# Kernel optimization log

Hardware: AMD Instinct MI355X
Metric: run time of the kernel (lower is better)

The kernel has to match this reference:

```python
import jax, jax.numpy as jnp
import numpy as np

N = 50000          # nodes
E = 600000         # edges
D = 128            # g_dim = h1_dim = h2_dim
R = 8              # 2 * n_speakers**2, n_speakers=2
B = 10             # num_bases


def setup_inputs() -> dict:
    key = jax.random.key(0)
    ks = jax.random.split(key, 10)
    s = 1.0 / np.sqrt(D)
    return {
        "node_features": jax.random.normal(ks[0], (N, D), jnp.float32),
        "edge_index": jax.random.randint(ks[1], (2, E), 0, N, jnp.int64),
        "edge_type": jax.random.randint(ks[2], (E,), 0, R, jnp.int64),
        # RGCNConv params (basis decomposition)
        "basis": jax.random.normal(ks[3], (B, D, D), jnp.float32) * s,
        "comp": jax.random.normal(ks[4], (R, B), jnp.float32) * (1.0 / np.sqrt(B)),
        "root": jax.random.normal(ks[5], (D, D), jnp.float32) * s,
        "bias1": jnp.zeros((D,), jnp.float32),
        # GraphConv params
        "w_rel": jax.random.normal(ks[6], (D, D), jnp.float32) * s,
        "b_rel": jnp.zeros((D,), jnp.float32),
        "w_root": jax.random.normal(ks[7], (D, D), jnp.float32) * s,
    }


def reference(node_features, edge_index, edge_type, basis, comp, root, bias1, w_rel, b_rel, w_root):
    x = node_features
    n = x.shape[0]
    r = comp.shape[0]
    src, dst = edge_index[0], edge_index[1]

    # ---- RGCNConv (basis decomposition, per-relation mean aggregation) ----
    # project through bases once: [N, B, D]
    xb = jnp.einsum('ni,bio->nbo', x, basis)
    # per-edge message: combine bases with relation coefficients  [E, D]
    msg = jnp.einsum('eb,ebo->eo', comp[edge_type], xb[src])
    # per-(dst, relation) mean normalization
    seg = dst * r + edge_type                       # [E]
    cnt = jax.ops.segment_sum(jnp.ones((msg.shape[0],), x.dtype), seg, num_segments=n * r)
    norm = 1.0 / jnp.maximum(cnt[seg], 1.0)         # [E]
    agg = jax.ops.segment_sum(msg * norm[:, None], dst, num_segments=n)  # [N, D]
    h1 = agg + x @ root + bias1

    # ---- GraphConv (add aggregation of neighbors + root transform) ----
    nbr = jax.ops.segment_sum(h1[src], dst, num_segments=n)  # [N, D]
    out = nbr @ w_rel.T + b_rel + h1 @ w_root.T
    return out
```

## Files before the change

kernel.cpp:

```cpp
#include <hip/hip_runtime.h>
#include <stdint.h>

#define N_NODES 50000
#define E_EDGES 600000
#define D 128
#define R_REL 8
#define B_BASES 10
#define RN (R_REL * N_NODES)

typedef __attribute__((ext_vector_type(8))) short bf16x8;
typedef __attribute__((ext_vector_type(4))) float f32x4;

__device__ __forceinline__ short f2b(float f) {
    uint32_t u = __float_as_uint(f);
    u += 0x7fff + ((u >> 16) & 1);
    return (short)(u >> 16);
}
__device__ __forceinline__ float b2f(uint16_t u) {
    return __uint_as_float((uint32_t)u << 16);
}

__global__ __launch_bounds__(256) void k_prep(const float* __restrict__ basis,
                                              const float* __restrict__ comp,
                                              const float* __restrict__ root,
                                              const float* __restrict__ wrel,
                                              const float* __restrict__ wroot,
                                              short* __restrict__ wt,
                                              short* __restrict__ wrel_b,
                                              short* __restrict__ wroot_b) {
    int tid = blockIdx.x * 256 + threadIdx.x;
    if (tid < 9 * D * D) {
        int s = tid >> 14;
        int rem = tid & 16383;
        int j = rem >> 7, i = rem & 127;
        float v;
        if (s < 8) {
            v = 0.f;
#pragma unroll
            for (int b = 0; b < B_BASES; b++)
                v += comp[s * B_BASES + b] * basis[b * D * D + i * D + j];
        } else {
            v = root[i * D + j];
        }
        wt[tid] = f2b(v);
    } else {
        int t2 = tid - 9 * D * D;
        if (t2 < D * D) {
            wrel_b[t2]  = f2b(wrel[t2]);
            wroot_b[t2] = f2b(wroot[t2]);
        }
    }
}

__global__ __launch_bounds__(256) void k_misc(const float* __restrict__ x,
                                              unsigned short* __restrict__ xb,
                                              const int* __restrict__ dst,
                                              const int* __restrict__ et,
                                              int* __restrict__ cntr) {
    int tid = blockIdx.x * 256 + threadIdx.x;
    if (tid < N_NODES * D / 8) {
        const float4* s = (const float4*)x + (size_t)tid * 2;
        float4 v0 = s[0], v1 = s[1];
        union { uint4 u; unsigned short h[8]; } pk;
        pk.h[0] = (unsigned short)f2b(v0.x); pk.h[1] = (unsigned short)f2b(v0.y);
        pk.h[2] = (unsigned short)f2b(v0.z); pk.h[3] = (unsigned short)f2b(v0.w);
        pk.h[4] = (unsigned short)f2b(v1.x); pk.h[5] = (unsigned short)f2b(v1.y);
        pk.h[6] = (unsigned short)f2b(v1.z); pk.h[7] = (unsigned short)f2b(v1.w);
        ((uint4*)xb)[tid] = pk.u;
    } else {
        int e = tid - N_NODES * D / 8;
        if (e < E_EDGES)
            atomicAdd(&cntr[dst[e] * R_REL + et[e]], 1);
    }
}

__device__ __forceinline__ int wave_scan_incl(int v) {
    int lane = threadIdx.x & 63;
#pragma unroll
    for (int off = 1; off < 64; off <<= 1) {
        int n = __shfl_up(v, off, 64);
        if (lane >= off) v += n;
    }
    return v;
}

__global__ __launch_bounds__(1024) void k_scan_a(const int* __restrict__ in,
                                                 int* __restrict__ out,
                                                 int* __restrict__ bsum, int n) {
    __shared__ int wsum[16];
    int t = threadIdx.x, lane = t & 63, wid = t >> 6;
    int g = blockIdx.x * 1024 + t;
    int v = (g < n) ? in[g] : 0;
    int isc = wave_scan_incl(v);
    if (lane == 63) wsum[wid] = isc;
    __syncthreads();
    if (wid == 0) {
        int wv = (lane < 16) ? wsum[lane] : 0;
        int wsc = wave_scan_incl(wv);
        if (lane < 16) wsum[lane] = wsc - wv;
    }
    __syncthreads();
    if (g < n) out[g] = wsum[wid] + isc - v;
    if (t == 1023 && bsum) bsum[blockIdx.x] = wsum[15] + isc;
}

__global__ __launch_bounds__(1024) void k_scan_c(int* __restrict__ out,
                                                 const int* __restrict__ bsum, int n) {
    int g = blockIdx.x * 1024 + threadIdx.x;
    if (g < n) out[g] += bsum[blockIdx.x];
}

__global__ __launch_bounds__(256) void k_bucket(const int* __restrict__ src,
                                                const int* __restrict__ dst,
                                                const int* __restrict__ et,
                                                const int* __restrict__ cntr,
                                                int* __restrict__ seg_off,
                                                int* __restrict__ es1,
                                                float* __restrict__ enorm) {
    int e = blockIdx.x * 256 + threadIdx.x;
    if (e >= E_EDGES) return;
    int r = et[e];
    int key = dst[e] * R_REL + r;
    int pos = atomicAdd(&seg_off[key], 1);
    es1[pos] = (src[e] << 3) | r;
    enorm[pos] = 1.0f / (float)cntr[key];
}

__global__ __launch_bounds__(256) void k_ygemm(const unsigned short* __restrict__ xb,
                                               const short* __restrict__ wt,
                                               unsigned short* __restrict__ ybig) {
    __shared__ short xs[64 * 128];
    __shared__ short ws[128 * 128];
    int slice = blockIdx.y;
    const short* w = wt + (size_t)slice * D * D;
    unsigned short* y = ybig + (size_t)slice * N_NODES * D;
    int base = blockIdx.x * 64;
    int t = threadIdx.x;
    const uint4* wsrc = (const uint4*)w;
    for (int idx = t; idx < 2048; idx += 256) {
        int j = idx >> 4, c = idx & 15;
        *(uint4*)&ws[j * 128 + ((c ^ (j & 15)) << 3)] = wsrc[idx];
    }
    for (int idx = t; idx < 1024; idx += 256) {
        int row = idx >> 4, c = idx & 15;
        int node = base + row;
        uint4 v = make_uint4(0, 0, 0, 0);
        if (node < N_NODES) v = ((const uint4*)(xb + (size_t)node * D))[c];
        *(uint4*)&xs[row * 128 + ((c ^ (row & 15)) << 3)] = v;
    }
    __syncthreads();

    int wave = t >> 6, lane = t & 63, quad = lane >> 4, l16 = lane & 15;
    f32x4 acc[8];
#pragma unroll
    for (int jt = 0; jt < 8; jt++) acc[jt] = (f32x4){0.f, 0.f, 0.f, 0.f};
#pragma unroll
    for (int kc = 0; kc < 4; kc++) {
        int c0 = kc * 4 + quad;
        bf16x8 a = *(const bf16x8*)&xs[(wave * 16 + l16) * 128 + ((c0 ^ l16) << 3)];
#pragma unroll
        for (int jt = 0; jt < 8; jt++) {
            bf16x8 b = *(const bf16x8*)&ws[(jt * 16 + l16) * 128 + ((c0 ^ l16) << 3)];
            acc[jt] = __builtin_amdgcn_mfma_f32_16x16x32_bf16(a, b, acc[jt], 0, 0, 0);
        }
    }
#pragma unroll
    for (int reg = 0; reg < 4; reg++) {
        int node = base + wave * 16 + quad * 4 + reg;
        if (node >= N_NODES) continue;
#pragma unroll
        for (int jt = 0; jt < 8; jt++)
            y[(size_t)node * D + jt * 16 + l16] = (unsigned short)f2b(acc[jt][reg]);
    }
}

__global__ __launch_bounds__(256) void k_agg8(const unsigned short* __restrict__ ybig,
                                              const int* __restrict__ es1,
                                              const float* __restrict__ enorm,
                                              const int* __restrict__ seg_off,
                                              const float* __restrict__ bias1,
                                              unsigned short* __restrict__ h1b) {
    int t = threadIdx.x;
    int wave = t >> 6, lane = t & 63, sub = lane >> 4, l = lane & 15;
    int d = blockIdx.x * 16 + wave * 4 + sub;
    if (d >= N_NODES) return;
    int start = (d == 0) ? 0 : seg_off[d * R_REL - 1];
    int end = seg_off[d * R_REL + 7];
    float acc[8];
#pragma unroll
    for (int j = 0; j < 8; j++) acc[j] = 0.f;
    size_t loff = (size_t)l * 8;

    int pos = start;
    for (; pos + 4 <= end; pos += 4) {
        int p0 = es1[pos], p1 = es1[pos + 1], p2 = es1[pos + 2], p3 = es1[pos + 3];
        float m0 = enorm[pos], m1 = enorm[pos + 1], m2 = enorm[pos + 2], m3 = enorm[pos + 3];
        uint4 v0 = *(const uint4*)(ybig + ((size_t)(p0 & 7) * N_NODES + (p0 >> 3)) * D + loff);
        uint4 v1 = *(const uint4*)(ybig + ((size_t)(p1 & 7) * N_NODES + (p1 >> 3)) * D + loff);
        uint4 v2 = *(const uint4*)(ybig + ((size_t)(p2 & 7) * N_NODES + (p2 >> 3)) * D + loff);
        uint4 v3 = *(const uint4*)(ybig + ((size_t)(p3 & 7) * N_NODES + (p3 >> 3)) * D + loff);
        const uint32_t* w0 = (const uint32_t*)&v0;
        const uint32_t* w1 = (const uint32_t*)&v1;
        const uint32_t* w2 = (const uint32_t*)&v2;
        const uint32_t* w3 = (const uint32_t*)&v3;
#pragma unroll
        for (int q = 0; q < 4; q++) {
            acc[q * 2]     += m0 * b2f((uint16_t)w0[q]) + m1 * b2f((uint16_t)w1[q]) +
                              m2 * b2f((uint16_t)w2[q]) + m3 * b2f((uint16_t)w3[q]);
            acc[q * 2 + 1] += m0 * b2f((uint16_t)(w0[q] >> 16)) + m1 * b2f((uint16_t)(w1[q] >> 16)) +
                              m2 * b2f((uint16_t)(w2[q] >> 16)) + m3 * b2f((uint16_t)(w3[q] >> 16));
        }
    }
    for (; pos < end; pos++) {
        int p0 = es1[pos];
        float m0 = enorm[pos];
        uint4 v0 = *(const uint4*)(ybig + ((size_t)(p0 & 7) * N_NODES + (p0 >> 3)) * D + loff);
        const uint32_t* w0 = (const uint32_t*)&v0;
#pragma unroll
        for (int q = 0; q < 4; q++) {
            acc[q * 2]     += m0 * b2f((uint16_t)w0[q]);
            acc[q * 2 + 1] += m0 * b2f((uint16_t)(w0[q] >> 16));
        }
    }

    uint4 rv = *(const uint4*)(ybig + ((size_t)8 * N_NODES + d) * D + loff);
    const uint32_t* rw = (const uint32_t*)&rv;
    float4 ba = *(const float4*)(bias1 + l * 8);
    float4 bb = *(const float4*)(bias1 + l * 8 + 4);
    float bv[8] = {ba.x, ba.y, ba.z, ba.w, bb.x, bb.y, bb.z, bb.w};
    union { uint4 u; unsigned short h[8]; } pk;
#pragma unroll
    for (int q = 0; q < 4; q++) {
        pk.h[q * 2]     = (unsigned short)f2b(acc[q * 2] + b2f((uint16_t)rw[q]) + bv[q * 2]);
        pk.h[q * 2 + 1] = (unsigned short)f2b(acc[q * 2 + 1] + b2f((uint16_t)(rw[q] >> 16)) + bv[q * 2 + 1]);
    }
    *(uint4*)(h1b + (size_t)d * D + loff) = pk.u;
}

__global__ __launch_bounds__(256) void k_agg_nbr(const unsigned short* __restrict__ h1b,
                                                 const int* __restrict__ es1,
                                                 const int* __restrict__ seg_off,
                                                 unsigned short* __restrict__ nbr) {
    int t = threadIdx.x;
    int wave = t >> 6, lane = t & 63, sub = lane >> 4, l = lane & 15;
    int d = blockIdx.x * 16 + wave * 4 + sub;
    if (d >= N_NODES) return;
    int start = (d == 0) ? 0 : seg_off[d * R_REL - 1];
    int end = seg_off[d * R_REL + 7];
    float acc[8];
#pragma unroll
    for (int j = 0; j < 8; j++) acc[j] = 0.f;
    size_t loff = (size_t)l * 8;

    int pos = start;
    for (; pos + 4 <= end; pos += 4) {
        int i0 = es1[pos] >> 3, i1 = es1[pos + 1] >> 3;
        int i2 = es1[pos + 2] >> 3, i3 = es1[pos + 3] >> 3;
        uint4 v0 = *(const uint4*)(h1b + (size_t)i0 * D + loff);
        uint4 v1 = *(const uint4*)(h1b + (size_t)i1 * D + loff);
        uint4 v2 = *(const uint4*)(h1b + (size_t)i2 * D + loff);
        uint4 v3 = *(const uint4*)(h1b + (size_t)i3 * D + loff);
        const uint32_t* w0 = (const uint32_t*)&v0;
        const uint32_t* w1 = (const uint32_t*)&v1;
        const uint32_t* w2 = (const uint32_t*)&v2;
        const uint32_t* w3 = (const uint32_t*)&v3;
#pragma unroll
        for (int q = 0; q < 4; q++) {
            acc[q * 2]     += b2f((uint16_t)w0[q]) + b2f((uint16_t)w1[q]) +
                              b2f((uint16_t)w2[q]) + b2f((uint16_t)w3[q]);
            acc[q * 2 + 1] += b2f((uint16_t)(w0[q] >> 16)) + b2f((uint16_t)(w1[q] >> 16)) +
                              b2f((uint16_t)(w2[q] >> 16)) + b2f((uint16_t)(w3[q] >> 16));
        }
    }
    for (; pos < end; pos++) {
        int i0 = es1[pos] >> 3;
        uint4 v0 = *(const uint4*)(h1b + (size_t)i0 * D + loff);
        const uint32_t* w0 = (const uint32_t*)&v0;
#pragma unroll
        for (int q = 0; q < 4; q++) {
            acc[q * 2]     += b2f((uint16_t)w0[q]);
            acc[q * 2 + 1] += b2f((uint16_t)(w0[q] >> 16));
        }
    }

    union { uint4 u; unsigned short h[8]; } pk;
#pragma unroll
    for (int j = 0; j < 8; j++) pk.h[j] = (unsigned short)f2b(acc[j]);
    *(uint4*)(nbr + (size_t)d * D + loff) = pk.u;
}

__global__ __launch_bounds__(256) void k_out2(const unsigned short* __restrict__ h1b,
                                              const unsigned short* __restrict__ nbr,
                                              const short* __restrict__ wroot_b,
                                              const short* __restrict__ wrel_b,
                                              const float* __restrict__ brel,
                                              float* __restrict__ out) {
    __shared__ short xs1[64 * 128];
    __shared__ short xs2[64 * 128];
    __shared__ short ws1[128 * 128];
    __shared__ short ws2[128 * 128];
    int base = blockIdx.x * 64;
    int t = threadIdx.x;
    const uint4* w1 = (const uint4*)wroot_b;
    const uint4* w2 = (const uint4*)wrel_b;
    for (int idx = t; idx < 2048; idx += 256) {
        int j = idx >> 4, c = idx & 15;
        int sw = j * 128 + ((c ^ (j & 15)) << 3);
        *(uint4*)&ws1[sw] = w1[idx];
        *(uint4*)&ws2[sw] = w2[idx];
    }
    for (int idx = t; idx < 1024; idx += 256) {
        int row = idx >> 4, c = idx & 15;
        int node = base + row;
        uint4 v1 = make_uint4(0, 0, 0, 0), v2 = make_uint4(0, 0, 0, 0);
        if (node < N_NODES) {
            v1 = ((const uint4*)(h1b + (size_t)node * D))[c];
            v2 = ((const uint4*)(nbr + (size_t)node * D))[c];
        }
        int sw = row * 128 + ((c ^ (row & 15)) << 3);
        *(uint4*)&xs1[sw] = v1;
        *(uint4*)&xs2[sw] = v2;
    }
    __syncthreads();

    int wave = t >> 6, lane = t & 63, quad = lane >> 4, l16 = lane & 15;
    f32x4 acc[8];
#pragma unroll
    for (int jt = 0; jt < 8; jt++) acc[jt] = (f32x4){0.f, 0.f, 0.f, 0.f};
#pragma unroll
    for (int kc = 0; kc < 4; kc++) {
        int c0 = kc * 4 + quad;
        int arow = (wave * 16 + l16) * 128 + ((c0 ^ l16) << 3);
        bf16x8 a1 = *(const bf16x8*)&xs1[arow];
        bf16x8 a2 = *(const bf16x8*)&xs2[arow];
#pragma unroll
        for (int jt = 0; jt < 8; jt++) {
            int brow = (jt * 16 + l16) * 128 + ((c0 ^ l16) << 3);
            bf16x8 b1 = *(const bf16x8*)&ws1[brow];
            bf16x8 b2 = *(const bf16x8*)&ws2[brow];
            acc[jt] = __builtin_amdgcn_mfma_f32_16x16x32_bf16(a1, b1, acc[jt], 0, 0, 0);
            acc[jt] = __builtin_amdgcn_mfma_f32_16x16x32_bf16(a2, b2, acc[jt], 0, 0, 0);
        }
    }
#pragma unroll
    for (int reg = 0; reg < 4; reg++) {
        int node = base + wave * 16 + quad * 4 + reg;
        if (node >= N_NODES) continue;
#pragma unroll
        for (int jt = 0; jt < 8; jt++) {
            int col = jt * 16 + l16;
            out[(size_t)node * D + col] = acc[jt][reg] + brel[col];
        }
    }
}

extern "C" void kernel_launch(void* const* d_in, const int* in_sizes, int n_in,
                              void* d_out, int out_size, void* d_ws, size_t ws_size,
                              hipStream_t stream) {
    const float* x     = (const float*)d_in[0];
    const int*   ei    = (const int*)d_in[1];
    const int*   et    = (const int*)d_in[2];
    const float* basis = (const float*)d_in[3];
    const float* comp  = (const float*)d_in[4];
    const float* root  = (const float*)d_in[5];
    const float* bias1 = (const float*)d_in[6];
    const float* wrel  = (const float*)d_in[7];
    const float* brel  = (const float*)d_in[8];
    const float* wroot = (const float*)d_in[9];
    float* out = (float*)d_out;
    const int* src = ei;
    const int* dst = ei + E_EDGES;

    char* p = (char*)d_ws;
    auto alloc = [&](size_t bytes) { char* q = p; p += (bytes + 255) & ~(size_t)255; return q; };
    short* wt      = (short*)alloc((size_t)9 * D * D * sizeof(short));
    short* wrel_b  = (short*)alloc(D * D * sizeof(short));
    short* wroot_b = (short*)alloc(D * D * sizeof(short));
    int*   cntr    = (int*)alloc((size_t)RN * sizeof(int));
    int*   seg_off = (int*)alloc((size_t)RN * sizeof(int));
    int*   es1     = (int*)alloc((size_t)(E_EDGES + 16) * sizeof(int));
    float* enorm   = (float*)alloc((size_t)(E_EDGES + 16) * sizeof(float));
    int*   bsum    = (int*)alloc(1024 * sizeof(int));
    unsigned short* xb   = (unsigned short*)alloc((size_t)N_NODES * D * sizeof(unsigned short));
    unsigned short* ybig = (unsigned short*)alloc((size_t)9 * N_NODES * D * sizeof(unsigned short));
    unsigned short* h1b  = (unsigned short*)alloc((size_t)N_NODES * D * sizeof(unsigned short));
    unsigned short* nbr  = xb;

    hipMemsetAsync(cntr, 0, (size_t)RN * sizeof(int), stream);

    k_prep<<<(9 * D * D + D * D + 255) / 256, 256, 0, stream>>>(
        basis, comp, root, wrel, wroot, wt, wrel_b, wroot_b);
    k_misc<<<(N_NODES * D / 8 + E_EDGES + 255) / 256, 256, 0, stream>>>(x, xb, dst, et, cntr);

    int nscan = (RN + 1023) / 1024;
    k_scan_a<<<nscan, 1024, 0, stream>>>(cntr, seg_off, bsum, RN);
    k_scan_a<<<1, 1024, 0, stream>>>(bsum, bsum, nullptr, nscan);
    k_scan_c<<<nscan, 1024, 0, stream>>>(seg_off, bsum, RN);

    k_bucket<<<(E_EDGES + 255) / 256, 256, 0, stream>>>(src, dst, et, cntr, seg_off, es1, enorm);

    int nb = (N_NODES + 63) / 64;
    int na = (N_NODES + 15) / 16;

    k_ygemm<<<dim3(nb, 9), 256, 0, stream>>>(xb, wt, ybig);
    k_agg8<<<na, 256, 0, stream>>>(ybig, es1, enorm, seg_off, bias1, h1b);
    k_agg_nbr<<<na, 256, 0, stream>>>(h1b, es1, seg_off, nbr);
    k_out2<<<nb, 256, 0, stream>>>(h1b, nbr, wroot_b, wrel_b, brel, out);
}
```

Before: 287.4 us.

## Aggregate before transform and fuse gather with MFMA GEMMs per node tile

Reorders the RGCN layer so that inputs are first mean-aggregated per relation, then each relation's weight is applied with MFMA inside one kernel. This removes the 9-slice projected tensor and its large write and read. The GraphConv neighbor sum is likewise fused into the output GEMM kernel, and the prep and misc launches are merged into one kernel. In exchange, each 64-node block gathers edges serially between GEMM passes and reloads a weight slice nine times, so memory latency and compute are less overlapped.

After: 348.7 us. 1.21x slower.

```diff
diff --git a/kernel.cpp b/kernel.cpp
--- a/kernel.cpp
+++ b/kernel.cpp
@@ -20,45 +20,22 @@
     return __uint_as_float((uint32_t)u << 16);
 }
 
-__global__ __launch_bounds__(256) void k_prep(const float* __restrict__ basis,
-                                              const float* __restrict__ comp,
-                                              const float* __restrict__ root,
-                                              const float* __restrict__ wrel,
-                                              const float* __restrict__ wroot,
-                                              short* __restrict__ wt,
-                                              short* __restrict__ wrel_b,
-                                              short* __restrict__ wroot_b) {
+__global__ __launch_bounds__(256) void k_front(const float* __restrict__ x,
+                                               unsigned short* __restrict__ xb,
+                                               const int* __restrict__ dst,
+                                               const int* __restrict__ et,
+                                               int* __restrict__ cntr,
+                                               const float* __restrict__ basis,
+                                               const float* __restrict__ comp,
+                                               const float* __restrict__ root,
+                                               const float* __restrict__ wrel,
+                                               const float* __restrict__ wroot,
+                                               short* __restrict__ wt,
+                                               short* __restrict__ wrel_b,
+                                               short* __restrict__ wroot_b) {
+    const int XB_N = N_NODES * D / 8;
     int tid = blockIdx.x * 256 + threadIdx.x;
-    if (tid < 9 * D * D) {
-        int s = tid >> 14;
-        int rem = tid & 16383;
-        int j = rem >> 7, i = rem & 127;
-        float v;
-        if (s < 8) {
-            v = 0.f;
-#pragma unroll
-            for (int b = 0; b < B_BASES; b++)
-                v += comp[s * B_BASES + b] * basis[b * D * D + i * D + j];
-        } else {
-            v = root[i * D + j];
-        }
-        wt[tid] = f2b(v);
-    } else {
-        int t2 = tid - 9 * D * D;
-        if (t2 < D * D) {
-            wrel_b[t2]  = f2b(wrel[t2]);
-            wroot_b[t2] = f2b(wroot[t2]);
-        }
-    }
-}
-
-__global__ __launch_bounds__(256) void k_misc(const float* __restrict__ x,
-                                              unsigned short* __restrict__ xb,
-                                              const int* __restrict__ dst,
-                                              const int* __restrict__ et,
-                                              int* __restrict__ cntr) {
-    int tid = blockIdx.x * 256 + threadIdx.x;
-    if (tid < N_NODES * D / 8) {
+    if (tid < XB_N) {
         const float4* s = (const float4*)x + (size_t)tid * 2;
         float4 v0 = s[0], v1 = s[1];
         union { uint4 u; unsigned short h[8]; } pk;
@@ -67,10 +44,32 @@
         pk.h[4] = (unsigned short)f2b(v1.x); pk.h[5] = (unsigned short)f2b(v1.y);
         pk.h[6] = (unsigned short)f2b(v1.z); pk.h[7] = (unsigned short)f2b(v1.w);
         ((uint4*)xb)[tid] = pk.u;
+    } else if (tid < XB_N + E_EDGES) {
+        int e = tid - XB_N;
+        atomicAdd(&cntr[dst[e] * R_REL + et[e]], 1);
     } else {
-        int e = tid - N_NODES * D / 8;
-        if (e < E_EDGES)
-            atomicAdd(&cntr[dst[e] * R_REL + et[e]], 1);
+        int t2 = tid - XB_N - E_EDGES;
+        if (t2 < 9 * D * D) {
+            int s = t2 >> 14;
+            int rem = t2 & 16383;
+            int j = rem >> 7, i = rem & 127;
+            float v;
+            if (s < 8) {
+                v = 0.f;
+#pragma unroll
+                for (int b = 0; b < B_BASES; b++)
+                    v += comp[s * B_BASES + b] * basis[b * D * D + i * D + j];
+            } else {
+                v = root[i * D + j];
+            }
+            wt[t2] = f2b(v);
+        } else {
+            int t3 = t2 - 9 * D * D;
+            if (t3 < D * D) {
+                wrel_b[t3]  = f2b(wrel[t3]);
+                wroot_b[t3] = f2b(wroot[t3]);
+            }
+        }
     }
 }
 
@@ -113,235 +112,213 @@
 __global__ __launch_bounds__(256) void k_bucket(const int* __restrict__ src,
                                                 const int* __restrict__ dst,
                                                 const int* __restrict__ et,
-                                                const int* __restrict__ cntr,
                                                 int* __restrict__ seg_off,
-                                                int* __restrict__ es1,
-                                                float* __restrict__ enorm) {
+                                                int* __restrict__ es1) {
     int e = blockIdx.x * 256 + threadIdx.x;
     if (e >= E_EDGES) return;
-    int r = et[e];
-    int key = dst[e] * R_REL + r;
+    int key = dst[e] * R_REL + et[e];
     int pos = atomicAdd(&seg_off[key], 1);
-    es1[pos] = (src[e] << 3) | r;
-    enorm[pos] = 1.0f / (float)cntr[key];
-}
-
-__global__ __launch_bounds__(256) void k_ygemm(const unsigned short* __restrict__ xb,
-                                               const short* __restrict__ wt,
-                                               unsigned short* __restrict__ ybig) {
+    es1[pos] = src[e];
+}
+
+__global__ __launch_bounds__(256) void k_h1_fused(const unsigned short* __restrict__ xb,
+                                                  const short* __restrict__ wt,
+                                                  const int* __restrict__ es1,
+                                                  const int* __restrict__ seg_off,
+                                                  const float* __restrict__ bias1,
+                                                  unsigned short* __restrict__ h1b) {
     __shared__ short xs[64 * 128];
     __shared__ short ws[128 * 128];
-    int slice = blockIdx.y;
-    const short* w = wt + (size_t)slice * D * D;
-    unsigned short* y = ybig + (size_t)slice * N_NODES * D;
+    __shared__ int sb[513];
     int base = blockIdx.x * 64;
     int t = threadIdx.x;
-    const uint4* wsrc = (const uint4*)w;
-    for (int idx = t; idx < 2048; idx += 256) {
-        int j = idx >> 4, c = idx & 15;
-        *(uint4*)&ws[j * 128 + ((c ^ (j & 15)) << 3)] = wsrc[idx];
-    }
-    for (int idx = t; idx < 1024; idx += 256) {
-        int row = idx >> 4, c = idx & 15;
-        int node = base + row;
-        uint4 v = make_uint4(0, 0, 0, 0);
-        if (node < N_NODES) v = ((const uint4*)(xb + (size_t)node * D))[c];
-        *(uint4*)&xs[row * 128 + ((c ^ (row & 15)) << 3)] = v;
-    }
-    __syncthreads();
+
+    for (int j = t; j < 513; j += 256) {
+        int g = base * 8 + j - 1;
+        sb[j] = (g < 0) ? 0 : seg_off[g < RN ? g : RN - 1];
+    }
 
     int wave = t >> 6, lane = t & 63, quad = lane >> 4, l16 = lane & 15;
+    int sw = t >> 4, l = t & 15;
     f32x4 acc[8];
 #pragma unroll
     for (int jt = 0; jt < 8; jt++) acc[jt] = (f32x4){0.f, 0.f, 0.f, 0.f};
-#pragma unroll
-    for (int kc = 0; kc < 4; kc++) {
-        int c0 = kc * 4 + quad;
-        bf16x8 a = *(const bf16x8*)&xs[(wave * 16 + l16) * 128 + ((c0 ^ l16) << 3)];
-#pragma unroll
-        for (int jt = 0; jt < 8; jt++) {
-            bf16x8 b = *(const bf16x8*)&ws[(jt * 16 + l16) * 128 + ((c0 ^ l16) << 3)];
-            acc[jt] = __builtin_amdgcn_mfma_f32_16x16x32_bf16(a, b, acc[jt], 0, 0, 0);
-        }
-    }
+
+    for (int r = 0; r < 9; r++) {
+        __syncthreads();
+        const uint4* wsrc = (const uint4*)(wt + (size_t)r * D * D);
+        for (int idx = t; idx < 2048; idx += 256) {
+            int j = idx >> 4, c = idx & 15;
+            *(uint4*)&ws[j * 128 + ((c ^ (j & 15)) << 3)] = wsrc[idx];
+        }
+        if (r < 8) {
+#pragma unroll
+            for (int ii = 0; ii < 4; ii++) {
+                int row = ii * 16 + sw;
+                int start = sb[row * 8 + r], end = sb[row * 8 + r + 1];
+                float ax[8];
+#pragma unroll
+                for (int q = 0; q < 8; q++) ax[q] = 0.f;
+                int pos = start;
+                for (; pos + 2 <= end; pos += 2) {
+                    int s0 = es1[pos], s1 = es1[pos + 1];
+                    uint4 v0 = *(const uint4*)(xb + (size_t)s0 * D + l * 8);
+                    uint4 v1 = *(const uint4*)(xb + (size_t)s1 * D + l * 8);
+                    const uint32_t* w0 = (const uint32_t*)&v0;
+                    const uint32_t* w1 = (const uint32_t*)&v1;
+#pragma unroll
+                    for (int q = 0; q < 4; q++) {
+                        ax[q * 2]     += b2f((uint16_t)w0[q]) + b2f((uint16_t)w1[q]);
+                        ax[q * 2 + 1] += b2f((uint16_t)(w0[q] >> 16)) + b2f((uint16_t)(w1[q] >> 16));
+                    }
+                }
+                if (pos < end) {
+                    int s0 = es1[pos];
+                    uint4 v0 = *(const uint4*)(xb + (size_t)s0 * D + l * 8);
+                    const uint32_t* w0 = (const uint32_t*)&v0;
+#pragma unroll
+                    for (int q = 0; q < 4; q++) {
+                        ax[q * 2]     += b2f((uint16_t)w0[q]);
+                        ax[q * 2 + 1] += b2f((uint16_t)(w0[q] >> 16));
+                    }
+                }
+                float nm = (end > start) ? 1.f / (float)(end - start) : 0.f;
+                union { uint4 u; unsigned short h[8]; } pk;
+#pragma unroll
+                for (int q = 0; q < 8; q++) pk.h[q] = (unsigned short)f2b(ax[q] * nm);
+                *(uint4*)&xs[row * 128 + ((l ^ (row & 15)) << 3)] = pk.u;
+            }
+        } else {
+            for (int idx = t; idx < 1024; idx += 256) {
+                int row = idx >> 4, c = idx & 15;
+                int node = base + row;
+                uint4 v = make_uint4(0, 0, 0, 0);
+                if (node < N_NODES) v = ((const uint4*)(xb + (size_t)node * D))[c];
+                *(uint4*)&xs[row * 128 + ((c ^ (row & 15)) << 3)] = v;
+            }
+        }
+        __syncthreads();
+#pragma unroll
+        for (int kc = 0; kc < 4; kc++) {
+            int c0 = kc * 4 + quad;
+            bf16x8 a = *(const bf16x8*)&xs[(wave * 16 + l16) * 128 + ((c0 ^ l16) << 3)];
+#pragma unroll
+            for (int jt = 0; jt < 8; jt++) {
+                bf16x8 b = *(const bf16x8*)&ws[(jt * 16 + l16) * 128 + ((c0 ^ l16) << 3)];
+                acc[jt] = __builtin_amdgcn_mfma_f32_16x16x32_bf16(a, b, acc[jt], 0, 0, 0);
+            }
+        }
+    }
+
 #pragma unroll
     for (int reg = 0; reg < 4; reg++) {
         int node = base + wave * 16 + quad * 4 + reg;
         if (node >= N_NODES) continue;
 #pragma unroll
-        for (int jt = 0; jt < 8; jt++)
-            y[(size_t)node * D + jt * 16 + l16] = (unsigned short)f2b(acc[jt][reg]);
-    }
-}
-
-__global__ __launch_bounds__(256) void k_agg8(const unsigned short* __restrict__ ybig,
-                                              const int* __restrict__ es1,
-                                              const float* __restrict__ enorm,
-                                              const int* __restrict__ seg_off,
-                                              const float* __restrict__ bias1,
-                                              unsigned short* __restrict__ h1b) {
-    int t = threadIdx.x;
-    int wave = t >> 6, lane = t & 63, sub = lane >> 4, l = lane & 15;
-    int d = blockIdx.x * 16 + wave * 4 + sub;
-    if (d >= N_NODES) return;
-    int start = (d == 0) ? 0 : seg_off[d * R_REL - 1];
-    int end = seg_off[d * R_REL + 7];
-    float acc[8];
-#pragma unroll
-    for (int j = 0; j < 8; j++) acc[j] = 0.f;
-    size_t loff = (size_t)l * 8;
-
-    int pos = start;
-    for (; pos + 4 <= end; pos += 4) {
-        int p0 = es1[pos], p1 = es1[pos + 1], p2 = es1[pos + 2], p3 = es1[pos + 3];
-        float m0 = enorm[pos], m1 = enorm[pos + 1], m2 = enorm[pos + 2], m3 = enorm[pos + 3];
-        uint4 v0 = *(const uint4*)(ybig + ((size_t)(p0 & 7) * N_NODES + (p0 >> 3)) * D + loff);
-        uint4 v1 = *(const uint4*)(ybig + ((size_t)(p1 & 7) * N_NODES + (p1 >> 3)) * D + loff);
-        uint4 v2 = *(const uint4*)(ybig + ((size_t)(p2 & 7) * N_NODES + (p2 >> 3)) * D + loff);
-        uint4 v3 = *(const uint4*)(ybig + ((size_t)(p3 & 7) * N_NODES + (p3 >> 3)) * D + loff);
-        const uint32_t* w0 = (const uint32_t*)&v0;
-        const uint32_t* w1 = (const uint32_t*)&v1;
-        const uint32_t* w2 = (const uint32_t*)&v2;
-        const uint32_t* w3 = (const uint32_t*)&v3;
-#pragma unroll
-        for (int q = 0; q < 4; q++) {
-            acc[q * 2]     += m0 * b2f((uint16_t)w0[q]) + m1 * b2f((uint16_t)w1[q]) +
-                              m2 * b2f((uint16_t)w2[q]) + m3 * b2f((uint16_t)w3[q]);
-            acc[q * 2 + 1] += m0 * b2f((uint16_t)(w0[q] >> 16)) + m1 * b2f((uint16_t)(w1[q] >> 16)) +
-                              m2 * b2f((uint16_t)(w2[q] >> 16)) + m3 * b2f((uint16_t)(w3[q] >> 16));
-        }
-    }
-    for (; pos < end; pos++) {
-        int p0 = es1[pos];
-        float m0 = enorm[pos];
-        uint4 v0 = *(const uint4*)(ybig + ((size_t)(p0 & 7) * N_NODES + (p0 >> 3)) * D + loff);
-        const uint32_t* w0 = (const uint32_t*)&v0;
-#pragma unroll
-        for (int q = 0; q < 4; q++) {
-            acc[q * 2]     += m0 * b2f((uint16_t)w0[q]);
-            acc[q * 2 + 1] += m0 * b2f((uint16_t)(w0[q] >> 16));
-        }
-    }
-
-    uint4 rv = *(const uint4*)(ybig + ((size_t)8 * N_NODES + d) * D + loff);
-    const uint32_t* rw = (const uint32_t*)&rv;
-    float4 ba = *(const float4*)(bias1 + l * 8);
-    float4 bb = *(const float4*)(bias1 + l * 8 + 4);
-    float bv[8] = {ba.x, ba.y, ba.z, ba.w, bb.x, bb.y, bb.z, bb.w};
-    union { uint4 u; unsigned short h[8]; } pk;
-#pragma unroll
-    for (int q = 0; q < 4; q++) {
-        pk.h[q * 2]     = (unsigned short)f2b(acc[q * 2] + b2f((uint16_t)rw[q]) + bv[q * 2]);
-        pk.h[q * 2 + 1] = (unsigned short)f2b(acc[q * 2 + 1] + b2f((uint16_t)(rw[q] >> 16)) + bv[q * 2 + 1]);
-    }
-    *(uint4*)(h1b + (size_t)d * D + loff) = pk.u;
-}
-
-__global__ __launch_bounds__(256) void k_agg_nbr(const unsigned short* __restrict__ h1b,
-                                                 const int* __restrict__ es1,
-                                                 const int* __restrict__ seg_off,
-                                                 unsigned short* __restrict__ nbr) {
-    int t = threadIdx.x;
-    int wave = t >> 6, lane = t & 63, sub = lane >> 4, l = lane & 15;
-    int d = blockIdx.x * 16 + wave * 4 + sub;
-    if (d >= N_NODES) return;
-    int start = (d == 0) ? 0 : seg_off[d * R_REL - 1];
-    int end = seg_off[d * R_REL + 7];
-    float acc[8];
-#pragma unroll
-    for (int j = 0; j < 8; j++) acc[j] = 0.f;
-    size_t loff = (size_t)l * 8;
-
-    int pos = start;
-    for (; pos + 4 <= end; pos += 4) {
-        int i0 = es1[pos] >> 3, i1 = es1[pos + 1] >> 3;
-        int i2 = es1[pos + 2] >> 3, i3 = es1[pos + 3] >> 3;
-        uint4 v0 = *(const uint4*)(h1b + (size_t)i0 * D + loff);
-        uint4 v1 = *(const uint4*)(h1b + (size_t)i1 * D + loff);
-        uint4 v2 = *(const uint4*)(h1b + (size_t)i2 * D + loff);
-        uint4 v3 = *(const uint4*)(h1b + (size_t)i3 * D + loff);
-        const uint32_t* w0 = (const uint32_t*)&v0;
-        const uint32_t* w1 = (const uint32_t*)&v1;
-        const uint32_t* w2 = (const uint32_t*)&v2;
-        const uint32_t* w3 = (const uint32_t*)&v3;
-#pragma unroll
-        for (int q = 0; q < 4; q++) {
-            acc[q * 2]     += b2f((uint16_t)w0[q]) + b2f((uint16_t)w1[q]) +
-                              b2f((uint16_t)w2[q]) + b2f((uint16_t)w3[q]);
-            acc[q * 2 + 1] += b2f((uint16_t)(w0[q] >> 16)) + b2f((uint16_t)(w1[q] >> 16)) +
-                              b2f((uint16_t)(w2[q] >> 16)) + b2f((uint16_t)(w3[q] >> 16));
-        }
-    }
-    for (; pos < end; pos++) {
-        int i0 = es1[pos] >> 3;
-        uint4 v0 = *(const uint4*)(h1b + (size_t)i0 * D + loff);
-        const uint32_t* w0 = (const uint32_t*)&v0;
-#pragma unroll
-        for (int q = 0; q < 4; q++) {
-            acc[q * 2]     += b2f((uint16_t)w0[q]);
-            acc[q * 2 + 1] += b2f((uint16_t)(w0[q] >> 16));
-        }
-    }
-
-    union { uint4 u; unsigned short h[8]; } pk;
-#pragma unroll
-    for (int j = 0; j < 8; j++) pk.h[j] = (unsigned short)f2b(acc[j]);
-    *(uint4*)(nbr + (size_t)d * D + loff) = pk.u;
-}
-
-__global__ __launch_bounds__(256) void k_out2(const unsigned short* __restrict__ h1b,
-                                              const unsigned short* __restrict__ nbr,
-                                              const short* __restrict__ wroot_b,
-                                              const short* __restrict__ wrel_b,
-                                              const float* __restrict__ brel,
-                                              float* __restrict__ out) {
-    __shared__ short xs1[64 * 128];
-    __shared__ short xs2[64 * 128];
-    __shared__ short ws1[128 * 128];
-    __shared__ short ws2[128 * 128];
+        for (int jt = 0; jt < 8; jt++) {
+            int col = jt * 16 + l16;
+            float v = acc[jt][reg] + bias1[col];
+            h1b[(size_t)node * D + col] = (unsigned short)f2b(v);
+        }
+    }
+}
+
+__global__ __launch_bounds__(256) void k_out_fused(const unsigned short* __restrict__ h1b,
+                                                   const int* __restrict__ es1,
+                                                   const int* __restrict__ seg_off,
+                                                   const short* __restrict__ wroot_b,
+                                                   const short* __restrict__ wrel_b,
+                                                   const float* __restrict__ brel,
+                                                   float* __restrict__ out) {
+    __shared__ short xs[64 * 128];
+    __shared__ short ws[128 * 128];
+    __shared__ int nbd[65];
     int base = blockIdx.x * 64;
     int t = threadIdx.x;
-    const uint4* w1 = (const uint4*)wroot_b;
-    const uint4* w2 = (const uint4*)wrel_b;
-    for (int idx = t; idx < 2048; idx += 256) {
-        int j = idx >> 4, c = idx & 15;
-        int sw = j * 128 + ((c ^ (j & 15)) << 3);
-        *(uint4*)&ws1[sw] = w1[idx];
-        *(uint4*)&ws2[sw] = w2[idx];
-    }
-    for (int idx = t; idx < 1024; idx += 256) {
-        int row = idx >> 4, c = idx & 15;
-        int node = base + row;
-        uint4 v1 = make_uint4(0, 0, 0, 0), v2 = make_uint4(0, 0, 0, 0);
-        if (node < N_NODES) {
-            v1 = ((const uint4*)(h1b + (size_t)node * D))[c];
-            v2 = ((const uint4*)(nbr + (size_t)node * D))[c];
-        }
-        int sw = row * 128 + ((c ^ (row & 15)) << 3);
-        *(uint4*)&xs1[sw] = v1;
-        *(uint4*)&xs2[sw] = v2;
-    }
-    __syncthreads();
+
+    for (int j = t; j < 65; j += 256) {
+        int g = (base + j) * 8 - 1;
+        nbd[j] = (g < 0) ? 0 : seg_off[g < RN ? g : RN - 1];
+    }
 
     int wave = t >> 6, lane = t & 63, quad = lane >> 4, l16 = lane & 15;
+    int sw = t >> 4, l = t & 15;
     f32x4 acc[8];
 #pragma unroll
     for (int jt = 0; jt < 8; jt++) acc[jt] = (f32x4){0.f, 0.f, 0.f, 0.f};
-#pragma unroll
-    for (int kc = 0; kc < 4; kc++) {
-        int c0 = kc * 4 + quad;
-        int arow = (wave * 16 + l16) * 128 + ((c0 ^ l16) << 3);
-        bf16x8 a1 = *(const bf16x8*)&xs1[arow];
-        bf16x8 a2 = *(const bf16x8*)&xs2[arow];
-#pragma unroll
-        for (int jt = 0; jt < 8; jt++) {
-            int brow = (jt * 16 + l16) * 128 + ((c0 ^ l16) << 3);
-            bf16x8 b1 = *(const bf16x8*)&ws1[brow];
-            bf16x8 b2 = *(const bf16x8*)&ws2[brow];
-            acc[jt] = __builtin_amdgcn_mfma_f32_16x16x32_bf16(a1, b1, acc[jt], 0, 0, 0);
-            acc[jt] = __builtin_amdgcn_mfma_f32_16x16x32_bf16(a2, b2, acc[jt], 0, 0, 0);
-        }
-    }
+
+    for (int pass = 0; pass < 2; pass++) {
+        __syncthreads();
+        const uint4* wsrc = (const uint4*)(pass == 0 ? wroot_b : wrel_b);
+        for (int idx = t; idx < 2048; idx += 256) {
+            int j = idx >> 4, c = idx & 15;
+            *(uint4*)&ws[j * 128 + ((c ^ (j & 15)) << 3)] = wsrc[idx];
+        }
+        if (pass == 0) {
+            for (int idx = t; idx < 1024; idx += 256) {
+                int row = idx >> 4, c = idx & 15;
+                int node = base + row;
+                uint4 v = make_uint4(0, 0, 0, 0);
+                if (node < N_NODES) v = ((const uint4*)(h1b + (size_t)node * D))[c];
+                *(uint4*)&xs[row * 128 + ((c ^ (row & 15)) << 3)] = v;
+            }
+        } else {
+#pragma unroll
+            for (int ii = 0; ii < 4; ii++) {
+                int row = ii * 16 + sw;
+                int start = nbd[row], end = nbd[row + 1];
+                float ax[8];
+#pragma unroll
+                for (int q = 0; q < 8; q++) ax[q] = 0.f;
+                int pos = start;
+                for (; pos + 4 <= end; pos += 4) {
+                    int s0 = es1[pos], s1 = es1[pos + 1];
+                    int s2 = es1[pos + 2], s3 = es1[pos + 3];
+                    uint4 v0 = *(const uint4*)(h1b + (size_t)s0 * D + l * 8);
+                    uint4 v1 = *(const uint4*)(h1b + (size_t)s1 * D + l * 8);
+                    uint4 v2 = *(const uint4*)(h1b + (size_t)s2 * D + l * 8);
+                    uint4 v3 = *(const uint4*)(h1b + (size_t)s3 * D + l * 8);
+                    const uint32_t* w0 = (const uint32_t*)&v0;
+                    const uint32_t* w1 = (const uint32_t*)&v1;
+                    const uint32_t* w2 = (const uint32_t*)&v2;
+                    const uint32_t* w3 = (const uint32_t*)&v3;
+#pragma unroll
+                    for (int q = 0; q < 4; q++) {
+                        ax[q * 2]     += b2f((uint16_t)w0[q]) + b2f((uint16_t)w1[q]) +
+                                         b2f((uint16_t)w2[q]) + b2f((uint16_t)w3[q]);
+                        ax[q * 2 + 1] += b2f((uint16_t)(w0[q] >> 16)) + b2f((uint16_t)(w1[q] >> 16)) +
+                                         b2f((uint16_t)(w2[q] >> 16)) + b2f((uint16_t)(w3[q] >> 16));
+                    }
+                }
+                for (; pos < end; pos++) {
+                    int s0 = es1[pos];
+                    uint4 v0 = *(const uint4*)(h1b + (size_t)s0 * D + l * 8);
+                    const uint32_t* w0 = (const uint32_t*)&v0;
+#pragma unroll
+                    for (int q = 0; q < 4; q++) {
+                        ax[q * 2]     += b2f((uint16_t)w0[q]);
+                        ax[q * 2 + 1] += b2f((uint16_t)(w0[q] >> 16));
+                    }
+                }
+                union { uint4 u; unsigned short h[8]; } pk;
+#pragma unroll
+                for (int q = 0; q < 8; q++) pk.h[q] = (unsigned short)f2b(ax[q]);
+                *(uint4*)&xs[row * 128 + ((l ^ (row & 15)) << 3)] = pk.u;
+            }
+        }
+        __syncthreads();
+#pragma unroll
+        for (int kc = 0; kc < 4; kc++) {
+            int c0 = kc * 4 + quad;
+            bf16x8 a = *(const bf16x8*)&xs[(wave * 16 + l16) * 128 + ((c0 ^ l16) << 3)];
+#pragma unroll
+            for (int jt = 0; jt < 8; jt++) {
+                bf16x8 b = *(const bf16x8*)&ws[(jt * 16 + l16) * 128 + ((c0 ^ l16) << 3)];
+                acc[jt] = __builtin_amdgcn_mfma_f32_16x16x32_bf16(a, b, acc[jt], 0, 0, 0);
+            }
+        }
+    }
+
 #pragma unroll
     for (int reg = 0; reg < 4; reg++) {
         int node = base + wave * 16 + quad * 4 + reg;
@@ -379,31 +356,26 @@
     int*   cntr    = (int*)alloc((size_t)RN * sizeof(int));
     int*   seg_off = (int*)alloc((size_t)RN * sizeof(int));
     int*   es1     = (int*)alloc((size_t)(E_EDGES + 16) * sizeof(int));
-    float* enorm   = (float*)alloc((size_t)(E_EDGES + 16) * sizeof(float));
     int*   bsum    = (int*)alloc(1024 * sizeof(int));
-    unsigned short* xb   = (unsigned short*)alloc((size_t)N_NODES * D * sizeof(unsigned short));
-    unsigned short* ybig = (unsigned short*)alloc((size_t)9 * N_NODES * D * sizeof(unsigned short));
-    unsigned short* h1b  = (unsigned short*)alloc((size_t)N_NODES * D * sizeof(unsigned short));
-    unsigned short* nbr  = xb;
+    unsigned short* xb  = (unsigned short*)alloc((size_t)N_NODES * D * sizeof(unsigned short));
+    unsigned short* h1b = (unsigned short*)alloc((size_t)N_NODES * D * sizeof(unsigned short));
 
     hipMemsetAsync(cntr, 0, (size_t)RN * sizeof(int), stream);
 
-    k_prep<<<(9 * D * D + D * D + 255) / 256, 256, 0, stream>>>(
-        basis, comp, root, wrel, wroot, wt, wrel_b, wroot_b);
-    k_misc<<<(N_NODES * D / 8 + E_EDGES + 255) / 256, 256, 0, stream>>>(x, xb, dst, et, cntr);
+    const int XB_N = N_NODES * D / 8;
+    int nfront = (XB_N + E_EDGES + 9 * D * D + D * D + 255) / 256;
+    k_front<<<nfront, 256, 0, stream>>>(x, xb, dst, et, cntr,
+                                        basis, comp, root, wrel, wroot,
+                                        wt, wrel_b, wroot_b);
 
     int nscan = (RN + 1023) / 1024;
     k_scan_a<<<nscan, 1024, 0, stream>>>(cntr, seg_off, bsum, RN);
     k_scan_a<<<1, 1024, 0, stream>>>(bsum, bsum, nullptr, nscan);
     k_scan_c<<<nscan, 1024, 0, stream>>>(seg_off, bsum, RN);
 
-    k_bucket<<<(E_EDGES + 255) / 256, 256, 0, stream>>>(src, dst, et, cntr, seg_off, es1, enorm);
+    k_bucket<<<(E_EDGES + 255) / 256, 256, 0, stream>>>(src, dst, et, seg_off, es1);
 
     int nb = (N_NODES + 63) / 64;
-    int na = (N_NODES + 15) / 16;
-
-    k_ygemm<<<dim3(nb, 9), 256, 0, stream>>>(xb, wt, ybig);
-    k_agg8<<<na, 256, 0, stream>>>(ybig, es1, enorm, seg_off, bias1, h1b);
-    k_agg_nbr<<<na, 256, 0, stream>>>(h1b, es1, seg_off, nbr);
-    k_out2<<<nb, 256, 0, stream>>>(h1b, nbr, wroot_b, wrel_b, brel, out);
-}
+    k_h1_fused<<<nb, 256, 0, stream>>>(xb, wt, es1, seg_off, bias1, h1b);
+    k_out_fused<<<nb, 256, 0, stream>>>(h1b, es1, seg_off, wroot_b, wrel_b, brel, out);
+}
```
